# Kernel optimization log

Hardware: AMD Instinct MI355X
Metric: run time of the kernel (lower is better)

The kernel has to match this reference:

```python
import jax, jax.numpy as jnp
import numpy as np

B, S, H = 1, 1024, 1024
E = 1024          # expert_dim
NEXP = 16         # num_experts
TOPK = 2
ALPHA = 1.702
LIMIT = 7.0


def setup_inputs() -> dict:
    key = jax.random.key(0)
    ks = jax.random.split(key, 8)
    hidden_states = jax.random.normal(ks[0], (B, S, H), dtype=jnp.float32)
    # router (gate): Linear(H, NEXP) with bias
    Wg = jax.random.normal(ks[1], (NEXP, H), dtype=jnp.float32) / np.sqrt(H)
    bg = jax.random.normal(ks[2], (NEXP,), dtype=jnp.float32) * 0.01
    # per-expert gate_up_proj: Linear(H, 2E) -> store as [NEXP, H, 2E]
    Wgu = jax.random.normal(ks[3], (NEXP, H, 2 * E), dtype=jnp.float32) / np.sqrt(H)
    bgu = jax.random.normal(ks[4], (NEXP, 2 * E), dtype=jnp.float32) * 0.01
    # per-expert down_proj: Linear(E, H) -> store as [NEXP, E, H]
    Wd = jax.random.normal(ks[5], (NEXP, E, H), dtype=jnp.float32) / np.sqrt(E)
    bd = jax.random.normal(ks[6], (NEXP, H), dtype=jnp.float32) * 0.01
    return {"hidden_states": hidden_states, "Wg": Wg, "bg": bg,
            "Wgu": Wgu, "bgu": bgu, "Wd": Wd, "bd": bd}


def _moe_forward(x, Wg, bg, Wgu, bgu, Wd, bd):
    b, s, h = x.shape
    xt = x.reshape(-1, h)                                   # [T, H]
    # router
    logits = xt @ Wg.T + bg                                 # [T, NEXP]
    # gpt_oss routing: topk over raw logits, softmax over selected
    top_vals, top_idx = jax.lax.top_k(logits, TOPK)         # [T, K]
    rw = jax.nn.softmax(top_vals.astype(jnp.float32), axis=-1).astype(xt.dtype)
    # combine weight per (token, expert): zero for unselected experts
    onehot = jax.nn.one_hot(top_idx, NEXP, dtype=xt.dtype)  # [T, K, NEXP]
    cw = jnp.einsum("tk,tke->te", rw, onehot)               # [T, NEXP]
    # dense expert compute (reference math identical to gather/scatter version)
    gu = jnp.einsum("th,ehf->tef", xt, Wgu) + bgu[None]     # [T, NEXP, 2E]
    gate = gu[..., ::2]
    up = gu[..., 1::2]
    gate = jnp.minimum(gate, LIMIT)
    up = jnp.clip(up, -LIMIT, LIMIT)
    glu = gate * jax.nn.sigmoid(gate * ALPHA)
    gated = (up + 1.0) * glu                                # [T, NEXP, E]
    out_e = jnp.einsum("tef,efh->teh", gated, Wd) + bd[None]  # [T, NEXP, H]
    out = jnp.einsum("teh,te->th", out_e, cw)               # [T, H]
    return out.reshape(b, s, h)


def reference(hidden_states, Wg, bg, Wgu, bgu, Wd, bd):
    return _moe_forward(hidden_states, Wg, bg, Wgu, bgu, Wd, bd)
```

## Files before the change

kernel.cpp:

```cpp
#include <hip/hip_runtime.h>
#include <hip/hip_bf16.h>

#define NT 1024
#define HD 1024
#define ED 1024
#define F2D 2048
#define NEXPERT 16
#define GROWS 2304
#define ALPHA_C 1.702f
#define LIMIT_C 7.0f

typedef float f32x4 __attribute__((ext_vector_type(4)));
typedef float fv4 __attribute__((ext_vector_type(4)));
typedef short short8 __attribute__((ext_vector_type(8)));
typedef unsigned int u32x4 __attribute__((ext_vector_type(4)));

__device__ __forceinline__ unsigned short f2bf(float x) {
  union { float f; unsigned int u; } v; v.f = x;
  unsigned int r = v.u + 0x7FFFu + ((v.u >> 16) & 1u);
  return (unsigned short)(r >> 16);
}
__device__ __forceinline__ unsigned int pk2(float lo, float hi) {
  return (unsigned int)f2bf(lo) | ((unsigned int)f2bf(hi) << 16);
}
__device__ __forceinline__ fv4 ldnt4(const float* p) {
  return __builtin_nontemporal_load((const fv4*)p);
}
__device__ __forceinline__ void async16(const void* g, void* l) {
  __builtin_amdgcn_global_load_lds((const __attribute__((address_space(1))) void*)g,
                                   (__attribute__((address_space(3))) void*)l, 16, 0, 0);
}

__global__ __launch_bounds__(64) void k_router(const float* __restrict__ x,
                                               const float* __restrict__ Wg,
                                               const float* __restrict__ bg,
                                               const float* __restrict__ bd,
                                               int* __restrict__ e01,
                                               float* __restrict__ w0f,
                                               float* __restrict__ w1f,
                                               unsigned short* __restrict__ Xbf,
                                               float* __restrict__ out) {
  const int t = blockIdx.x;
  const int l = threadIdx.x;
  const float4* x4 = (const float4*)(x + (size_t)t * HD);
  for (int i = 0; i < 4; ++i) {
    const int idx = l + 64 * i;
    float4 v = x4[idx];
    unsigned int a = pk2(v.x, v.y);
    unsigned int b = pk2(v.z, v.w);
    unsigned int* dst = (unsigned int*)(Xbf + (size_t)t * HD + idx * 4);
    dst[0] = a; dst[1] = b;
  }
  const int e = l & 15, qq = l >> 4;
  const float4* wg4 = (const float4*)(Wg + (size_t)e * HD);
  float s = 0.f;
  for (int j = 0; j < 64; ++j) {
    const int idx = qq + 4 * j;
    float4 a = x4[idx], b = wg4[idx];
    s += a.x * b.x + a.y * b.y + a.z * b.z + a.w * b.w;
  }
  s += __shfl_xor(s, 16);
  s += __shfl_xor(s, 32);
  const float logit = s + bg[e];
  float v0 = -1e30f, v1 = -1e30f; int i0 = 0, i1 = 0;
  for (int k = 0; k < 16; ++k) {
    float lv = __shfl(logit, k);
    if (lv > v0) { v1 = v0; i1 = i0; v0 = lv; i0 = k; }
    else if (lv > v1) { v1 = lv; i1 = k; }
  }
  const float w0 = 1.f / (1.f + __expf(v1 - v0));
  const float w1 = 1.f - w0;
  if (l == 0) {
    e01[t] = i0 | (i1 << 8);
    w0f[t] = w0;
    w1f[t] = w1;
  }
  const float4* bd0 = (const float4*)(bd + (size_t)i0 * HD);
  const float4* bd1 = (const float4*)(bd + (size_t)i1 * HD);
  float4* o4 = (float4*)(out + (size_t)t * HD);
  for (int i = 0; i < 4; ++i) {
    const int idx = l + 64 * i;
    float4 a = bd0[idx], b = bd1[idx];
    float4 r;
    r.x = w0 * a.x + w1 * b.x;
    r.y = w0 * a.y + w1 * b.y;
    r.z = w0 * a.z + w1 * b.z;
    r.w = w0 * a.w + w1 * b.w;
    o4[idx] = r;
  }
}

__global__ __launch_bounds__(1024) void k_scan(const int* __restrict__ e01,
                                               const float* __restrict__ w0f,
                                               const float* __restrict__ w1f,
                                               int* __restrict__ cnt,
                                               int* __restrict__ off,
                                               int* __restrict__ gtok,
                                               float* __restrict__ gwt) {
  __shared__ int scnt[NEXPERT];
  __shared__ int soff[NEXPERT];
  __shared__ int scur[NEXPERT];
  const int t = threadIdx.x;
  if (t < NEXPERT) { scnt[t] = 0; scur[t] = 0; }
  __syncthreads();
  const int p = e01[t];
  const int e0 = p & 255, e1 = p >> 8;
  atomicAdd(&scnt[e0], 1);
  atomicAdd(&scnt[e1], 1);
  __syncthreads();
  if (t == 0) {
    int a = 0;
    for (int e = 0; e < NEXPERT; ++e) { soff[e] = a; off[e] = a; cnt[e] = scnt[e]; a += scnt[e]; }
  }
  __syncthreads();
  int s0 = atomicAdd(&scur[e0], 1);
  gtok[soff[e0] + s0] = t; gwt[soff[e0] + s0] = w0f[t];
  int s1 = atomicAdd(&scur[e1], 1);
  gtok[soff[e1] + s1] = t; gwt[soff[e1] + s1] = w1f[t];
}

#define BSTG1 132
__global__ __launch_bounds__(512, 2) void k_gemm1(const unsigned short* __restrict__ Xbf,
                                                  const float* __restrict__ Wgu,
                                                  const float* __restrict__ bgu,
                                                  const int* __restrict__ cnt,
                                                  const int* __restrict__ off,
                                                  const int* __restrict__ gtok,
                                                  unsigned short* __restrict__ Gact) {
  const int e = blockIdx.z;
  const int Ne = cnt[e];
  const int mtile = blockIdx.y;
  if (mtile * 256 >= Ne) return;
  const int ntile = blockIdx.x;
  const int tid = threadIdx.x;
  const int lane = tid & 63;
  const int wv = tid >> 6;
  const int wm = wv >> 1;
  const int wn = wv & 1;
  const int q = lane >> 4;
  const int fr = lane & 15;
  const int base = off[e] + mtile * 256;

  __shared__ unsigned short Alds[2][256 * 32];
  __shared__ unsigned int Blds[2][16 * BSTG1];

  const int ar0 = wv * 32 + (lane >> 2);
  const int ar1 = ar0 + 16;
  const int ags0 = base + (((mtile * 256 + ar0) < Ne) ? ar0 : 0);
  const int ags1 = base + (((mtile * 256 + ar1) < Ne) ? ar1 : 0);
  const unsigned short* agp0 = Xbf + (size_t)gtok[ags0] * HD + (lane & 3) * 8;
  const unsigned short* agp1 = Xbf + (size_t)gtok[ags1] * HD + (lane & 3) * 8;
  const int aofs = wv * 1024;

  const int p2 = tid >> 5;
  const int bc = tid & 31;
  const float* Wb = Wgu + (size_t)e * HD * F2D + (size_t)(2 * p2) * F2D + ntile * 128 + bc * 4;

  f32x4 acc[4][4] = {};
  fv4 b0, b1;

  b0 = ldnt4(Wb);
  b1 = ldnt4(Wb + F2D);
  async16(agp0, Alds[0] + aofs);
  async16(agp1, Alds[0] + aofs + 512);
  {
    u32x4 pkv;
    pkv[0] = pk2(b0[0], b1[0]); pkv[1] = pk2(b0[1], b1[1]);
    pkv[2] = pk2(b0[2], b1[2]); pkv[3] = pk2(b0[3], b1[3]);
    *(u32x4*)(Blds[0] + p2 * BSTG1 + bc * 4) = pkv;
  }
  __syncthreads();

  for (int ks = 0; ks < 32; ++ks) {
    const int cur = ks & 1, nxt = cur ^ 1;
    const bool more = (ks + 1) < 32;
    if (more) {
      const float* bp = Wb + (size_t)(ks + 1) * 32 * F2D;
      b0 = ldnt4(bp);
      b1 = ldnt4(bp + F2D);
      async16(agp0 + (ks + 1) * 32, Alds[nxt] + aofs);
      async16(agp1 + (ks + 1) * 32, Alds[nxt] + aofs + 512);
    }
    short8 af[4], bfr[4];
#pragma unroll
    for (int mi = 0; mi < 4; ++mi)
      af[mi] = *(const short8*)(Alds[cur] + (wm * 64 + mi * 16 + fr) * 32 + q * 8);
#pragma unroll
    for (int ni = 0; ni < 4; ++ni) {
      const unsigned int* p = Blds[cur] + (q * 4) * BSTG1 + wn * 64 + ni * 16 + fr;
      union { unsigned int u[4]; short8 s; } uu;
      uu.u[0] = p[0]; uu.u[1] = p[BSTG1]; uu.u[2] = p[2 * BSTG1]; uu.u[3] = p[3 * BSTG1];
      bfr[ni] = uu.s;
    }
#pragma unroll
    for (int mi = 0; mi < 4; ++mi)
#pragma unroll
      for (int ni = 0; ni < 4; ++ni)
        acc[mi][ni] = __builtin_amdgcn_mfma_f32_16x16x32_bf16(af[mi], bfr[ni], acc[mi][ni], 0, 0, 0);
    if (more) {
      u32x4 pkv;
      pkv[0] = pk2(b0[0], b1[0]); pkv[1] = pk2(b0[1], b1[1]);
      pkv[2] = pk2(b0[2], b1[2]); pkv[3] = pk2(b0[3], b1[3]);
      *(u32x4*)(Blds[nxt] + p2 * BSTG1 + bc * 4) = pkv;
    }
    __syncthreads();
  }

  const float* bguE = bgu + (size_t)e * F2D + ntile * 128;
#pragma unroll
  for (int mi = 0; mi < 4; ++mi) {
#pragma unroll
    for (int ni = 0; ni < 4; ++ni) {
      const int coll = wn * 64 + ni * 16 + fr;
      const float bias = bguE[coll];
#pragma unroll
      for (int r = 0; r < 4; ++r) {
        const int srow = wm * 64 + mi * 16 + q * 4 + r;
        float v = acc[mi][ni][r] + bias;
        float pv = __shfl_xor(v, 1);
        float gate = (lane & 1) ? pv : v;
        float up   = (lane & 1) ? v : pv;
        gate = fminf(gate, LIMIT_C);
        up = fminf(fmaxf(up, -LIMIT_C), LIMIT_C);
        float glu = gate / (1.f + __expf(-ALPHA_C * gate));
        float val = (up + 1.f) * glu;
        if (!(lane & 1) && (mtile * 256 + srow) < Ne)
          Gact[(size_t)(base + srow) * ED + ((ntile * 128 + coll) >> 1)] = f2bf(val);
      }
    }
  }
}

#define BSTG2 68
__global__ __launch_bounds__(256, 2) void k_gemm2(const unsigned short* __restrict__ Gact,
                                                  const float* __restrict__ Wd,
                                                  const int* __restrict__ cnt,
                                                  const int* __restrict__ off,
                                                  const int* __restrict__ gtok,
                                                  const float* __restrict__ gwt,
                                                  float* __restrict__ out) {
  const int e = blockIdx.z;
  const int Ne = cnt[e];
  const int mtile = blockIdx.y;
  if (mtile * 256 >= Ne) return;
  const int ntile = blockIdx.x;
  const int tid = threadIdx.x;
  const int lane = tid & 63;
  const int wv = tid >> 6;
  const int q = lane >> 4;
  const int fr = lane & 15;
  const int base = off[e] + mtile * 256;

  __shared__ unsigned short Alds[2][256 * 32];
  __shared__ unsigned int Blds[2][16 * BSTG2];

  const int arb = wv * 64 + (lane >> 2);
  const unsigned short* agp = Gact + (size_t)(base + arb) * ED + (lane & 3) * 8;
  const int aofs = wv * 2048;

  const int p2 = tid >> 4;
  const int bc = tid & 15;
  const float* Wb = Wd + (size_t)e * ED * HD + (size_t)(2 * p2) * HD + ntile * 64 + bc * 4;

  f32x4 acc[4][4] = {};
  fv4 b0, b1;

  b0 = ldnt4(Wb);
  b1 = ldnt4(Wb + HD);
#pragma unroll
  for (int j = 0; j < 4; ++j)
    async16(agp + (size_t)j * 16 * ED, Alds[0] + aofs + j * 512);
  {
    u32x4 pkv;
    pkv[0] = pk2(b0[0], b1[0]); pkv[1] = pk2(b0[1], b1[1]);
    pkv[2] = pk2(b0[2], b1[2]); pkv[3] = pk2(b0[3], b1[3]);
    *(u32x4*)(Blds[0] + p2 * BSTG2 + bc * 4) = pkv;
  }
  __syncthreads();

  for (int ks = 0; ks < 32; ++ks) {
    const int cur = ks & 1, nxt = cur ^ 1;
    const bool more = (ks + 1) < 32;
    if (more) {
      const float* bp = Wb + (size_t)(ks + 1) * 32 * HD;
      b0 = ldnt4(bp);
      b1 = ldnt4(bp + HD);
#pragma unroll
      for (int j = 0; j < 4; ++j)
        async16(agp + (ks + 1) * 32 + (size_t)j * 16 * ED, Alds[nxt] + aofs + j * 512);
    }
    short8 af[4], bfr[4];
#pragma unroll
    for (int mi = 0; mi < 4; ++mi)
      af[mi] = *(const short8*)(Alds[cur] + (wv * 64 + mi * 16 + fr) * 32 + q * 8);
#pragma unroll
    for (int ni = 0; ni < 4; ++ni) {
      const unsigned int* p = Blds[cur] + (q * 4) * BSTG2 + ni * 16 + fr;
      union { unsigned int u[4]; short8 s; } uu;
      uu.u[0] = p[0]; uu.u[1] = p[BSTG2]; uu.u[2] = p[2 * BSTG2]; uu.u[3] = p[3 * BSTG2];
      bfr[ni] = uu.s;
    }
#pragma unroll
    for (int mi = 0; mi < 4; ++mi)
#pragma unroll
      for (int ni = 0; ni < 4; ++ni)
        acc[mi][ni] = __builtin_amdgcn_mfma_f32_16x16x32_bf16(af[mi], bfr[ni], acc[mi][ni], 0, 0, 0);
    if (more) {
      u32x4 pkv;
      pkv[0] = pk2(b0[0], b1[0]); pkv[1] = pk2(b0[1], b1[1]);
      pkv[2] = pk2(b0[2], b1[2]); pkv[3] = pk2(b0[3], b1[3]);
      *(u32x4*)(Blds[nxt] + p2 * BSTG2 + bc * 4) = pkv;
    }
    __syncthreads();
  }

#pragma unroll
  for (int mi = 0; mi < 4; ++mi) {
#pragma unroll
    for (int r = 0; r < 4; ++r) {
      const int srow = wv * 64 + mi * 16 + q * 4 + r;
      if ((mtile * 256 + srow) < Ne) {
        const int gsl = base + srow;
        const int tok = gtok[gsl];
        const float wt = gwt[gsl];
        float* op = out + (size_t)tok * HD + ntile * 64;
#pragma unroll
        for (int ni = 0; ni < 4; ++ni) {
          const int col = ni * 16 + fr;
          atomicAdd(op + col, wt * acc[mi][ni][r]);
        }
      }
    }
  }
}

extern "C" void kernel_launch(void* const* d_in, const int* in_sizes, int n_in,
                              void* d_out, int out_size, void* d_ws, size_t ws_size,
                              hipStream_t stream) {
  const float* x   = (const float*)d_in[0];
  const float* Wg  = (const float*)d_in[1];
  const float* bg  = (const float*)d_in[2];
  const float* Wgu = (const float*)d_in[3];
  const float* bgu = (const float*)d_in[4];
  const float* Wd  = (const float*)d_in[5];
  const float* bd  = (const float*)d_in[6];
  float* out = (float*)d_out;

  int* cnt = (int*)d_ws;
  int* off = cnt + 16;
  int* e01 = off + 16;
  float* w0f = (float*)(e01 + NT);
  float* w1f = w0f + NT;
  int* gtok = (int*)(w1f + NT);
  float* gwt = (float*)(gtok + GROWS);
  unsigned short* Xbf = (unsigned short*)(gwt + GROWS);
  unsigned short* Gact = Xbf + (size_t)NT * HD;

  k_router<<<NT, 64, 0, stream>>>(x, Wg, bg, bd, e01, w0f, w1f, Xbf, out);
  k_scan<<<1, NT, 0, stream>>>(e01, w0f, w1f, cnt, off, gtok, gwt);
  k_gemm1<<<dim3(16, 2, NEXPERT), 512, 0, stream>>>(Xbf, Wgu, bgu, cnt, off, gtok, Gact);
  k_gemm2<<<dim3(16, 2, NEXPERT), 256, 0, stream>>>(Gact, Wd, cnt, off, gtok, gwt, out);
}
```

Before: 340.7 us.

## Replace atomic scatter in down-proj with per-slot stores plus combine kernel

The down-projection kernel now writes each routed row's result to a per-slot buffer with plain stores instead of atomically adding weighted values into the output. A new combine kernel gathers each token's two slot rows, adds expert biases, and applies routing weights, taking over bias initialization from the router. The router dot product is split into two accumulators, and gemm1's launch bounds drop to one block per CU. This removes atomic contention at the cost of an extra kernel launch and a roughly 9 MB intermediate round trip.

```diff
diff --git a/kernel.cpp b/kernel.cpp
--- a/kernel.cpp
+++ b/kernel.cpp
@@ -34,12 +34,10 @@
 __global__ __launch_bounds__(64) void k_router(const float* __restrict__ x,
                                                const float* __restrict__ Wg,
                                                const float* __restrict__ bg,
-                                               const float* __restrict__ bd,
                                                int* __restrict__ e01,
                                                float* __restrict__ w0f,
                                                float* __restrict__ w1f,
-                                               unsigned short* __restrict__ Xbf,
-                                               float* __restrict__ out) {
+                                               unsigned short* __restrict__ Xbf) {
   const int t = blockIdx.x;
   const int l = threadIdx.x;
   const float4* x4 = (const float4*)(x + (size_t)t * HD);
@@ -53,12 +51,17 @@
   }
   const int e = l & 15, qq = l >> 4;
   const float4* wg4 = (const float4*)(Wg + (size_t)e * HD);
-  float s = 0.f;
-  for (int j = 0; j < 64; ++j) {
-    const int idx = qq + 4 * j;
-    float4 a = x4[idx], b = wg4[idx];
-    s += a.x * b.x + a.y * b.y + a.z * b.z + a.w * b.w;
-  }
+  float s0a = 0.f, s1a = 0.f;
+#pragma unroll 8
+  for (int j = 0; j < 32; ++j) {
+    const int i0 = qq + 8 * j;
+    const int i1 = i0 + 4;
+    float4 a0 = x4[i0], b0 = wg4[i0];
+    float4 a1 = x4[i1], b1 = wg4[i1];
+    s0a += a0.x * b0.x + a0.y * b0.y + a0.z * b0.z + a0.w * b0.w;
+    s1a += a1.x * b1.x + a1.y * b1.y + a1.z * b1.z + a1.w * b1.w;
+  }
+  float s = s0a + s1a;
   s += __shfl_xor(s, 16);
   s += __shfl_xor(s, 32);
   const float logit = s + bg[e];
@@ -75,28 +78,13 @@
     w0f[t] = w0;
     w1f[t] = w1;
   }
-  const float4* bd0 = (const float4*)(bd + (size_t)i0 * HD);
-  const float4* bd1 = (const float4*)(bd + (size_t)i1 * HD);
-  float4* o4 = (float4*)(out + (size_t)t * HD);
-  for (int i = 0; i < 4; ++i) {
-    const int idx = l + 64 * i;
-    float4 a = bd0[idx], b = bd1[idx];
-    float4 r;
-    r.x = w0 * a.x + w1 * b.x;
-    r.y = w0 * a.y + w1 * b.y;
-    r.z = w0 * a.z + w1 * b.z;
-    r.w = w0 * a.w + w1 * b.w;
-    o4[idx] = r;
-  }
 }
 
 __global__ __launch_bounds__(1024) void k_scan(const int* __restrict__ e01,
-                                               const float* __restrict__ w0f,
-                                               const float* __restrict__ w1f,
                                                int* __restrict__ cnt,
                                                int* __restrict__ off,
                                                int* __restrict__ gtok,
-                                               float* __restrict__ gwt) {
+                                               int* __restrict__ sl01) {
   __shared__ int scnt[NEXPERT];
   __shared__ int soff[NEXPERT];
   __shared__ int scur[NEXPERT];
@@ -114,13 +102,16 @@
   }
   __syncthreads();
   int s0 = atomicAdd(&scur[e0], 1);
-  gtok[soff[e0] + s0] = t; gwt[soff[e0] + s0] = w0f[t];
+  const int g0 = soff[e0] + s0;
+  gtok[g0] = t;
   int s1 = atomicAdd(&scur[e1], 1);
-  gtok[soff[e1] + s1] = t; gwt[soff[e1] + s1] = w1f[t];
+  const int g1 = soff[e1] + s1;
+  gtok[g1] = t;
+  sl01[t] = g0 | (g1 << 16);
 }
 
 #define BSTG1 132
-__global__ __launch_bounds__(512, 2) void k_gemm1(const unsigned short* __restrict__ Xbf,
+__global__ __launch_bounds__(512, 1) void k_gemm1(const unsigned short* __restrict__ Xbf,
                                                   const float* __restrict__ Wgu,
                                                   const float* __restrict__ bgu,
                                                   const int* __restrict__ cnt,
@@ -236,9 +227,7 @@
                                                   const float* __restrict__ Wd,
                                                   const int* __restrict__ cnt,
                                                   const int* __restrict__ off,
-                                                  const int* __restrict__ gtok,
-                                                  const float* __restrict__ gwt,
-                                                  float* __restrict__ out) {
+                                                  float* __restrict__ Oe) {
   const int e = blockIdx.z;
   const int Ne = cnt[e];
   const int mtile = blockIdx.y;
@@ -320,18 +309,39 @@
     for (int r = 0; r < 4; ++r) {
       const int srow = wv * 64 + mi * 16 + q * 4 + r;
       if ((mtile * 256 + srow) < Ne) {
-        const int gsl = base + srow;
-        const int tok = gtok[gsl];
-        const float wt = gwt[gsl];
-        float* op = out + (size_t)tok * HD + ntile * 64;
-#pragma unroll
-        for (int ni = 0; ni < 4; ++ni) {
-          const int col = ni * 16 + fr;
-          atomicAdd(op + col, wt * acc[mi][ni][r]);
-        }
+        float* op = Oe + (size_t)(base + srow) * HD + ntile * 64;
+#pragma unroll
+        for (int ni = 0; ni < 4; ++ni)
+          op[ni * 16 + fr] = acc[mi][ni][r];
       }
     }
   }
+}
+
+__global__ __launch_bounds__(256) void k_combine(const float* __restrict__ Oe,
+                                                 const float* __restrict__ bd,
+                                                 const int* __restrict__ e01,
+                                                 const int* __restrict__ sl01,
+                                                 const float* __restrict__ w0f,
+                                                 const float* __restrict__ w1f,
+                                                 float* __restrict__ out) {
+  const int t = blockIdx.x;
+  const int i = threadIdx.x;
+  const int p = e01[t];
+  const int e0 = p & 255, e1 = p >> 8;
+  const int sl = sl01[t];
+  const int s0 = sl & 0xFFFF, s1 = (sl >> 16) & 0xFFFF;
+  const float w0 = w0f[t], w1 = w1f[t];
+  float4 a = ((const float4*)(Oe + (size_t)s0 * HD))[i];
+  float4 b = ((const float4*)(Oe + (size_t)s1 * HD))[i];
+  float4 c = ((const float4*)(bd + (size_t)e0 * HD))[i];
+  float4 d = ((const float4*)(bd + (size_t)e1 * HD))[i];
+  float4 r;
+  r.x = w0 * (a.x + c.x) + w1 * (b.x + d.x);
+  r.y = w0 * (a.y + c.y) + w1 * (b.y + d.y);
+  r.z = w0 * (a.z + c.z) + w1 * (b.z + d.z);
+  r.w = w0 * (a.w + c.w) + w1 * (b.w + d.w);
+  ((float4*)(out + (size_t)t * HD))[i] = r;
 }
 
 extern "C" void kernel_launch(void* const* d_in, const int* in_sizes, int n_in,
@@ -349,15 +359,17 @@
   int* cnt = (int*)d_ws;
   int* off = cnt + 16;
   int* e01 = off + 16;
-  float* w0f = (float*)(e01 + NT);
+  int* sl01 = e01 + NT;
+  float* w0f = (float*)(sl01 + NT);
   float* w1f = w0f + NT;
   int* gtok = (int*)(w1f + NT);
-  float* gwt = (float*)(gtok + GROWS);
-  unsigned short* Xbf = (unsigned short*)(gwt + GROWS);
+  float* Oe = (float*)(gtok + GROWS);
+  unsigned short* Xbf = (unsigned short*)(Oe + (size_t)GROWS * HD);
   unsigned short* Gact = Xbf + (size_t)NT * HD;
 
-  k_router<<<NT, 64, 0, stream>>>(x, Wg, bg, bd, e01, w0f, w1f, Xbf, out);
-  k_scan<<<1, NT, 0, stream>>>(e01, w0f, w1f, cnt, off, gtok, gwt);
+  k_router<<<NT, 64, 0, stream>>>(x, Wg, bg, e01, w0f, w1f, Xbf);
+  k_scan<<<1, NT, 0, stream>>>(e01, cnt, off, gtok, sl01);
   k_gemm1<<<dim3(16, 2, NEXPERT), 512, 0, stream>>>(Xbf, Wgu, bgu, cnt, off, gtok, Gact);
-  k_gemm2<<<dim3(16, 2, NEXPERT), 256, 0, stream>>>(Gact, Wd, cnt, off, gtok, gwt, out);
-}
+  k_gemm2<<<dim3(16, 2, NEXPERT), 256, 0, stream>>>(Gact, Wd, cnt, off, Oe);
+  k_combine<<<NT, 256, 0, stream>>>(Oe, bd, e01, sl01, w0f, w1f, out);
+}
```

Result: no change. 343.5 us (+0.8%).

## Double gemm2 warps per block, split router dot into two accumulators, relax gemm1 bounds

Applied to the files above, without the earlier changes.

The down-projection kernel now runs 8 waves per block, each covering 32 rows instead of 64, which halves per-wave accumulators and A-tile loads. Only the first 256 threads load and pack the B tile. The router's dot product uses two independent accumulators with unrolling to add memory-level parallelism. gemm1's launch bounds drop to one block per CU, giving the compiler more registers at the cost of occupancy.

```diff
diff --git a/kernel.cpp b/kernel.cpp
--- a/kernel.cpp
+++ b/kernel.cpp
@@ -53,12 +53,17 @@
   }
   const int e = l & 15, qq = l >> 4;
   const float4* wg4 = (const float4*)(Wg + (size_t)e * HD);
-  float s = 0.f;
-  for (int j = 0; j < 64; ++j) {
-    const int idx = qq + 4 * j;
-    float4 a = x4[idx], b = wg4[idx];
-    s += a.x * b.x + a.y * b.y + a.z * b.z + a.w * b.w;
-  }
+  float s0a = 0.f, s1a = 0.f;
+#pragma unroll 8
+  for (int j = 0; j < 32; ++j) {
+    const int i0 = qq + 8 * j;
+    const int i1 = i0 + 4;
+    float4 a0 = x4[i0], b0 = wg4[i0];
+    float4 a1 = x4[i1], b1 = wg4[i1];
+    s0a += a0.x * b0.x + a0.y * b0.y + a0.z * b0.z + a0.w * b0.w;
+    s1a += a1.x * b1.x + a1.y * b1.y + a1.z * b1.z + a1.w * b1.w;
+  }
+  float s = s0a + s1a;
   s += __shfl_xor(s, 16);
   s += __shfl_xor(s, 32);
   const float logit = s + bg[e];
@@ -120,7 +125,7 @@
 }
 
 #define BSTG1 132
-__global__ __launch_bounds__(512, 2) void k_gemm1(const unsigned short* __restrict__ Xbf,
+__global__ __launch_bounds__(512, 1) void k_gemm1(const unsigned short* __restrict__ Xbf,
                                                   const float* __restrict__ Wgu,
                                                   const float* __restrict__ bgu,
                                                   const int* __restrict__ cnt,
@@ -232,7 +237,7 @@
 }
 
 #define BSTG2 68
-__global__ __launch_bounds__(256, 2) void k_gemm2(const unsigned short* __restrict__ Gact,
+__global__ __launch_bounds__(512, 2) void k_gemm2(const unsigned short* __restrict__ Gact,
                                                   const float* __restrict__ Wd,
                                                   const int* __restrict__ cnt,
                                                   const int* __restrict__ off,
@@ -254,23 +259,25 @@
   __shared__ unsigned short Alds[2][256 * 32];
   __shared__ unsigned int Blds[2][16 * BSTG2];
 
-  const int arb = wv * 64 + (lane >> 2);
-  const unsigned short* agp = Gact + (size_t)(base + arb) * ED + (lane & 3) * 8;
-  const int aofs = wv * 2048;
+  const int ar0 = wv * 32 + (lane >> 2);
+  const unsigned short* agp0 = Gact + (size_t)(base + ar0) * ED + (lane & 3) * 8;
+  const unsigned short* agp1 = agp0 + (size_t)16 * ED;
+  const int aofs = wv * 1024;
 
   const int p2 = tid >> 4;
   const int bc = tid & 15;
   const float* Wb = Wd + (size_t)e * ED * HD + (size_t)(2 * p2) * HD + ntile * 64 + bc * 4;
 
-  f32x4 acc[4][4] = {};
+  f32x4 acc[2][4] = {};
   fv4 b0, b1;
 
-  b0 = ldnt4(Wb);
-  b1 = ldnt4(Wb + HD);
-#pragma unroll
-  for (int j = 0; j < 4; ++j)
-    async16(agp + (size_t)j * 16 * ED, Alds[0] + aofs + j * 512);
-  {
+  if (tid < 256) {
+    b0 = ldnt4(Wb);
+    b1 = ldnt4(Wb + HD);
+  }
+  async16(agp0, Alds[0] + aofs);
+  async16(agp1, Alds[0] + aofs + 512);
+  if (tid < 256) {
     u32x4 pkv;
     pkv[0] = pk2(b0[0], b1[0]); pkv[1] = pk2(b0[1], b1[1]);
     pkv[2] = pk2(b0[2], b1[2]); pkv[3] = pk2(b0[3], b1[3]);
@@ -282,17 +289,18 @@
     const int cur = ks & 1, nxt = cur ^ 1;
     const bool more = (ks + 1) < 32;
     if (more) {
-      const float* bp = Wb + (size_t)(ks + 1) * 32 * HD;
-      b0 = ldnt4(bp);
-      b1 = ldnt4(bp + HD);
-#pragma unroll
-      for (int j = 0; j < 4; ++j)
-        async16(agp + (ks + 1) * 32 + (size_t)j * 16 * ED, Alds[nxt] + aofs + j * 512);
-    }
-    short8 af[4], bfr[4];
-#pragma unroll
-    for (int mi = 0; mi < 4; ++mi)
-      af[mi] = *(const short8*)(Alds[cur] + (wv * 64 + mi * 16 + fr) * 32 + q * 8);
+      if (tid < 256) {
+        const float* bp = Wb + (size_t)(ks + 1) * 32 * HD;
+        b0 = ldnt4(bp);
+        b1 = ldnt4(bp + HD);
+      }
+      async16(agp0 + (ks + 1) * 32, Alds[nxt] + aofs);
+      async16(agp1 + (ks + 1) * 32, Alds[nxt] + aofs + 512);
+    }
+    short8 af[2], bfr[4];
+#pragma unroll
+    for (int mi = 0; mi < 2; ++mi)
+      af[mi] = *(const short8*)(Alds[cur] + (wv * 32 + mi * 16 + fr) * 32 + q * 8);
 #pragma unroll
     for (int ni = 0; ni < 4; ++ni) {
       const unsigned int* p = Blds[cur] + (q * 4) * BSTG2 + ni * 16 + fr;
@@ -301,11 +309,11 @@
       bfr[ni] = uu.s;
     }
 #pragma unroll
-    for (int mi = 0; mi < 4; ++mi)
+    for (int mi = 0; mi < 2; ++mi)
 #pragma unroll
       for (int ni = 0; ni < 4; ++ni)
         acc[mi][ni] = __builtin_amdgcn_mfma_f32_16x16x32_bf16(af[mi], bfr[ni], acc[mi][ni], 0, 0, 0);
-    if (more) {
+    if (more && tid < 256) {
       u32x4 pkv;
       pkv[0] = pk2(b0[0], b1[0]); pkv[1] = pk2(b0[1], b1[1]);
       pkv[2] = pk2(b0[2], b1[2]); pkv[3] = pk2(b0[3], b1[3]);
@@ -315,10 +323,10 @@
   }
 
 #pragma unroll
-  for (int mi = 0; mi < 4; ++mi) {
+  for (int mi = 0; mi < 2; ++mi) {
 #pragma unroll
     for (int r = 0; r < 4; ++r) {
-      const int srow = wv * 64 + mi * 16 + q * 4 + r;
+      const int srow = wv * 32 + mi * 16 + q * 4 + r;
       if ((mtile * 256 + srow) < Ne) {
         const int gsl = base + srow;
         const int tok = gtok[gsl];
@@ -359,5 +367,5 @@
   k_router<<<NT, 64, 0, stream>>>(x, Wg, bg, bd, e01, w0f, w1f, Xbf, out);
   k_scan<<<1, NT, 0, stream>>>(e01, w0f, w1f, cnt, off, gtok, gwt);
   k_gemm1<<<dim3(16, 2, NEXPERT), 512, 0, stream>>>(Xbf, Wgu, bgu, cnt, off, gtok, Gact);
-  k_gemm2<<<dim3(16, 2, NEXPERT), 256, 0, stream>>>(Gact, Wd, cnt, off, gtok, gwt, out);
-}
+  k_gemm2<<<dim3(16, 2, NEXPERT), 512, 0, stream>>>(Gact, Wd, cnt, off, gtok, gwt, out);
+}
```

Result: faster. 332.4 us (-2.4%).
